# Kernel optimization log

Hardware: AMD Instinct MI355X
Metric: run time of the kernel (lower is better)

Reference implementation:

```python
import jax, jax.numpy as jnp
import numpy as np

V, H, FAST, SLOW = 32000, 256, 64, 256
B, T = 32, 1024
THRESH = 0.3
NEG = -1e9


def setup_inputs() -> dict:
    key = jax.random.key(0)
    ks = jax.random.split(key, 16)
    s = 0.02
    return {
        "seq":   jax.random.randint(ks[0], (B, T), 0, V),
        "embed": jax.random.normal(ks[1], (V, H), jnp.float32) * s,
        "W1": jax.random.normal(ks[2], (H, 2 * H), jnp.float32) * s,
        "b1": jnp.zeros((2 * H,), jnp.float32),
        "W2": jax.random.normal(ks[3], (2 * H, H), jnp.float32) * s,
        "b2": jnp.zeros((H,), jnp.float32),
        "gamma": jnp.ones((H,), jnp.float32),
        "beta":  jnp.zeros((H,), jnp.float32),
        "Wg": jax.random.normal(ks[4], (H, 1), jnp.float32) * s,
        "bg": jnp.zeros((1,), jnp.float32),
        "Wd": jax.random.normal(ks[5], (H, 1), jnp.float32) * s,
        "bd": jnp.zeros((1,), jnp.float32),
        "Wq": jax.random.normal(ks[6], (H, H), jnp.float32) * s,
        "bq": jnp.zeros((H,), jnp.float32),
        "Wo": jax.random.normal(ks[7], (H, V), jnp.float32) * s,
        "bo": jnp.zeros((V,), jnp.float32),
    }


def _layer_norm(x, g, b, eps=1e-5):
    mu = x.mean(-1, keepdims=True)
    var = ((x - mu) ** 2).mean(-1, keepdims=True)
    return (x - mu) * jax.lax.rsqrt(var + eps) * g + b


def _writer(h, Wg, bg, Wd, bd):
    """Vectorized-over-batch LRU writer with learned demotion; scan over time."""
    Bn = h.shape[0]
    init = (
        jnp.zeros((Bn, FAST, H), h.dtype),   # fast_mem
        jnp.zeros((Bn, SLOW, H), h.dtype),   # slow_mem
        jnp.zeros((Bn, FAST), jnp.int32),    # fast_age
        jnp.zeros((Bn, SLOW), jnp.int32),    # slow_age
        jnp.zeros((Bn, FAST), bool),         # fast_used
        jnp.zeros((Bn, SLOW), bool),         # slow_used
    )

    def step(st, tok_h):
        fm, sm, fa, sa, fu, su = st
        ws = jax.nn.sigmoid(tok_h @ Wg + bg)[:, 0]          # [B]
        fa = fa + fu.astype(jnp.int32)
        sa = sa + su.astype(jnp.int32)
        write = ws >= 0.4                                    # torch skips if < 0.4
        tok = jax.lax.stop_gradient(tok_h)                   # .detach() in torch

        free_f = ~fu                                         # [B,FAST]
        has_free = jnp.any(free_f, axis=1)                   # [B]
        sl = jnp.argmax(free_f, axis=1)                      # first free fast slot

        ds = (fm @ Wd + bd)[..., 0]                          # [B,FAST] demotion scores
        dem = jnp.argmin(ds, axis=1)                         # [B]
        dh = jnp.take_along_axis(fm, dem[:, None, None], axis=1)[:, 0]  # [B,H]

        free_s = ~su
        has_free_s = jnp.any(free_s, axis=1)
        ss = jnp.where(has_free_s, jnp.argmax(free_s, axis=1), jnp.argmax(sa, axis=1))

        fidx = jnp.where(has_free, sl, dem)                  # fast write slot
        sel_f = jax.nn.one_hot(fidx, FAST, dtype=bool) & write[:, None]
        do_slow = write & ~has_free                          # demotion happens
        sel_s = jax.nn.one_hot(ss, SLOW, dtype=bool) & do_slow[:, None]

        # slow write (demoted value) uses fm BEFORE the fast overwrite
        sm = jnp.where(sel_s[:, :, None], dh[:, None, :], sm)
        sa = jnp.where(sel_s, 0, sa)
        su = su | sel_s

        fm = jnp.where(sel_f[:, :, None], tok[:, None, :], fm)
        fa = jnp.where(sel_f, 0, fa)
        fu = fu | sel_f
        return (fm, sm, fa, sa, fu, su), None

    tokens = jnp.swapaxes(h[:, : h.shape[1] - 3], 0, 1)      # [T-3, B, H]
    (fm, sm, fa, sa, fu, su), _ = jax.lax.scan(step, init, tokens)
    return fm, sm, fu.astype(h.dtype), su.astype(h.dtype)


def reference(seq, embed, W1, b1, W2, b2, gamma, beta, Wg, bg, Wd, bd, Wq, bq, Wo, bo):
    h0 = embed[seq]                                          # [B,T,H]
    ff = jnp.maximum(h0 @ W1 + b1, 0.0) @ W2 + b2
    h = _layer_norm(h0 + ff, gamma, beta)

    fm, sm, fmask, smask = _writer(h, Wg, bg, Wd, bd)

    q = h[:, -1, :] @ Wq + bq                                # [B,H]
    f_scores = jnp.einsum("bfd,bd->bf", fm, q)
    f_scores = jnp.where(fmask == 0, NEG, f_scores)
    f_attn = jax.nn.softmax(f_scores, axis=-1)
    f_ctx = jnp.einsum("bf,bfd->bd", f_attn, fm)
    max_attn = f_attn.max(axis=-1)

    s_scores = jnp.einsum("bsd,bd->bs", sm, q)
    s_scores = jnp.where(smask == 0, NEG, s_scores)
    s_attn = jax.nn.softmax(s_scores, axis=-1)
    s_ctx = jnp.einsum("bs,bsd->bd", s_attn, sm)

    need_slow = (max_attn < THRESH).astype(h.dtype)          # [B]
    ctx = f_ctx + need_slow[:, None] * s_ctx
    logits = ctx @ Wo + bo
    return logits, need_slow
```

## Files before the change

### kernel.cpp

```cpp
#include <hip/hip_runtime.h>
#include <hip/hip_bf16.h>
#include <cstdint>

#define NEGV -1e9f

typedef __attribute__((ext_vector_type(8))) short short8v;
typedef __attribute__((ext_vector_type(4))) float f32x4;

union U8 {
  unsigned u[4];
  short8v v;
};

__device__ __forceinline__ float wred_sum(float v) {
#pragma unroll
  for (int o = 32; o; o >>= 1) v += __shfl_xor(v, o);
  return v;
}
__device__ __forceinline__ float wred_max(float v) {
#pragma unroll
  for (int o = 32; o; o >>= 1) v = fmaxf(v, __shfl_xor(v, o));
  return v;
}
template <int CTRL>
__device__ __forceinline__ float dpp_fadd(float x) {
  int xi = __float_as_int(x);
  int yi = __builtin_amdgcn_update_dpp(xi, xi, CTRL, 0xF, 0xF, false);
  return x + __int_as_float(yi);
}
__device__ __forceinline__ float dpp_sum63(float v) {
  v = dpp_fadd<0xB1>(v);
  v = dpp_fadd<0x4E>(v);
  v = dpp_fadd<0x141>(v);
  v = dpp_fadd<0x140>(v);
  v = dpp_fadd<0x142>(v);
  v = dpp_fadd<0x143>(v);
  return v;
}
__device__ __forceinline__ float dpp_sum16(float v) {
  v = dpp_fadd<0xB1>(v);
  v = dpp_fadd<0x4E>(v);
  v = dpp_fadd<0x141>(v);
  v = dpp_fadd<0x140>(v);
  return v;
}

__device__ __forceinline__ ushort bf16hi(float x) {
  unsigned u = __float_as_uint(x);
  unsigned r = u + 0x7FFFu + ((u >> 16) & 1u);
  return (ushort)(r >> 16);
}
__device__ __forceinline__ float bf16tof(ushort u) {
  return __uint_as_float(((unsigned)u) << 16);
}
__device__ __forceinline__ void split8(const float* xs, uint4& hv, uint4& lv) {
  unsigned h[8], l[8];
#pragma unroll
  for (int j = 0; j < 8; ++j) {
    const ushort hh = bf16hi(xs[j]);
    h[j] = hh;
    l[j] = bf16hi(xs[j] - bf16tof(hh));
  }
  hv = make_uint4(h[0] | (h[1] << 16), h[2] | (h[3] << 16),
                  h[4] | (h[5] << 16), h[6] | (h[7] << 16));
  lv = make_uint4(l[0] | (l[1] << 16), l[2] | (l[3] << 16),
                  l[4] | (l[5] << 16), l[6] | (l[7] << 16));
}

__device__ __forceinline__ void gload_lds16(const void* g, void* l) {
  __builtin_amdgcn_global_load_lds(
      (const __attribute__((address_space(1))) unsigned int*)g,
      (__attribute__((address_space(3))) unsigned int*)l, 16, 0, 0);
}

__global__ __launch_bounds__(256) void wprep2_k(const float* __restrict__ W,
                                                char* __restrict__ Wti, int K,
                                                int N) {
  __shared__ float tile[32][33];
  const int k0 = blockIdx.x * 32, n0 = blockIdx.y * 32;
  const int r = threadIdx.x >> 5, c = threadIdx.x & 31;
#pragma unroll
  for (int i = 0; i < 4; ++i)
    tile[r + i * 8][c] = W[(size_t)(k0 + r + i * 8) * N + n0 + c];
  __syncthreads();
  if (threadIdx.x < 128) {
    const int gn = threadIdx.x & 31, gk = threadIdx.x >> 5;
    float xs[8];
#pragma unroll
    for (int i = 0; i < 8; ++i) xs[i] = tile[gk * 8 + i][gn];
    uint4 hv, lv;
    split8(xs, hv, lv);
    char* dst = Wti + (size_t)(n0 + gn) * K * 4 + (k0 >> 5) * 128 + gk * 16;
    *(uint4*)dst = hv;
    *(uint4*)(dst + 64) = lv;
  }
}

__global__ __launch_bounds__(512, 2) void gemm1g_k(
    const int* __restrict__ seq, const float* __restrict__ embed,
    const char* __restrict__ w1ti, const float* __restrict__ bias,
    unsigned* __restrict__ outp) {
  __shared__ alignas(16) ushort A[4096];
  __shared__ alignas(16) ushort B[16384];
  __shared__ int sidx[64];
  const int tid = threadIdx.x;
  const int m0 = blockIdx.x * 64, n0 = blockIdx.y * 256;
  if (tid < 64) sidx[tid] = seq[m0 + tid];
  __syncthreads();
  const int lane = tid & 63, w = tid >> 6;
  const int wm = (w >> 2) * 32, wn = (w & 3) * 64;
  const int r15 = lane & 15, khalf = lane >> 4;

  f32x4 acc[2][4];
#pragma unroll
  for (int i = 0; i < 2; ++i)
#pragma unroll
    for (int j = 0; j < 4; ++j) acc[i][j] = (f32x4){0.f, 0.f, 0.f, 0.f};

#pragma unroll 1
  for (int s = 0; s < 8; ++s) {
    const size_t sb = (size_t)s * 128;
    if (tid < 256) {
      const int row = tid >> 2, q = tid & 3;
      const float* ap = embed + (size_t)sidx[row] * 256 + s * 32 + q * 8;
      const float4 x0 = *(const float4*)ap;
      const float4 x1 = *(const float4*)(ap + 4);
      const float xs[8] = {x0.x, x0.y, x0.z, x0.w, x1.x, x1.y, x1.z, x1.w};
      uint4 hv, lv;
      split8(xs, hv, lv);
      const int r7 = row & 7;
      *(uint4*)&A[(row * 8 + (q ^ r7)) * 8] = hv;
      *(uint4*)&A[(row * 8 + ((4 | q) ^ r7)) * 8] = lv;
    }
#pragma unroll
    for (int i = 0; i < 4; ++i) {
      const int cb = i * 512 + w * 64;
      const int c = cb + lane;
      const int row = c >> 3;
      const int lc = (c & 7) ^ (row & 7);
      gload_lds16(w1ti + (size_t)(n0 + row) * 1024 + sb + lc * 16,
                  &B[cb * 8]);
    }
    __syncthreads();
    short8v ahf[2], alf[2], bhf[4], blf[4];
#pragma unroll
    for (int t = 0; t < 2; ++t) {
      const int ra = wm + t * 16 + r15;
      ahf[t] = *(const short8v*)&A[(ra * 8 + (khalf ^ (ra & 7))) * 8];
      alf[t] = *(const short8v*)&A[(ra * 8 + ((4 | khalf) ^ (ra & 7))) * 8];
    }
#pragma unroll
    for (int t = 0; t < 4; ++t) {
      const int rb = wn + t * 16 + r15;
      bhf[t] = *(const short8v*)&B[(rb * 8 + (khalf ^ (rb & 7))) * 8];
      blf[t] = *(const short8v*)&B[(rb * 8 + ((4 | khalf) ^ (rb & 7))) * 8];
    }
#pragma unroll
    for (int mi = 0; mi < 2; ++mi)
#pragma unroll
      for (int ni = 0; ni < 4; ++ni) {
        acc[mi][ni] = __builtin_amdgcn_mfma_f32_16x16x32_bf16(
            ahf[mi], bhf[ni], acc[mi][ni], 0, 0, 0);
        acc[mi][ni] = __builtin_amdgcn_mfma_f32_16x16x32_bf16(
            ahf[mi], blf[ni], acc[mi][ni], 0, 0, 0);
        acc[mi][ni] = __builtin_amdgcn_mfma_f32_16x16x32_bf16(
            alf[mi], bhf[ni], acc[mi][ni], 0, 0, 0);
      }
    __syncthreads();
  }
#pragma unroll
  for (int ni = 0; ni < 4; ++ni) {
    const int n = n0 + wn + ni * 16 + r15;
    const float bv = bias[n];
#pragma unroll
    for (int mi = 0; mi < 2; ++mi) {
      const int mbase = m0 + wm + mi * 16 + khalf * 4;
#pragma unroll
      for (int j = 0; j < 4; ++j) {
        const float t = fmaxf(acc[mi][ni][j] + bv, 0.f);
        const ushort h = bf16hi(t);
        const ushort l = bf16hi(t - bf16tof(h));
        outp[(size_t)(mbase + j) * 512 + n] = (unsigned)h | ((unsigned)l << 16);
      }
    }
  }
}

__global__ __launch_bounds__(512, 2) void gemm2i_k(
    const unsigned* __restrict__ Ap, const char* __restrict__ w2ti,
    const float* __restrict__ b2, const int* __restrict__ seq,
    const float* __restrict__ embed, const float* __restrict__ gamma,
    const float* __restrict__ beta, const float* __restrict__ Wg,
    const float* __restrict__ bg, const float* __restrict__ Wd,
    const float* __restrict__ bd, float* __restrict__ X,
    int* __restrict__ wbit, float* __restrict__ dsc) {
  __shared__ alignas(16) unsigned Apk[2048];
  __shared__ alignas(16) ushort B[16384];
  __shared__ float par0[64][4], par1[64][4], gpar[64][4], dpar[64][4];
  __shared__ float g_s[256], be_s[256], wg_s[256], wd_s[256], b2_s[256];
  __shared__ int sidx[64];
  const int tid = threadIdx.x;
  const int m0 = blockIdx.x * 64;
  if (tid < 64) sidx[tid] = seq[m0 + tid];
  if (tid >= 256) {
    const int c = tid - 256;
    g_s[c] = gamma[c];
    be_s[c] = beta[c];
    wg_s[c] = Wg[c];
    wd_s[c] = Wd[c];
    b2_s[c] = b2[c];
  }
  const int lane = tid & 63, w = tid >> 6;
  const int wm = (w >> 2) * 32, wn = (w & 3) * 64;
  const int r15 = lane & 15, khalf = lane >> 4;

  f32x4 acc[2][4];
#pragma unroll
  for (int i = 0; i < 2; ++i)
#pragma unroll
    for (int j = 0; j < 4; ++j) acc[i][j] = (f32x4){0.f, 0.f, 0.f, 0.f};

#pragma unroll 1
  for (int s = 0; s < 16; ++s) {
    {
      const int cb = w * 64;
      const int c = cb + lane;
      const int row = c >> 3;
      const int lc = (c & 7) ^ (row & 7);
      gload_lds16(Ap + (size_t)(m0 + row) * 512 + s * 32 + lc * 4,
                  &Apk[cb * 4]);
    }
    const size_t sb = (size_t)s * 128;
#pragma unroll
    for (int i = 0; i < 4; ++i) {
      const int cb = i * 512 + w * 64;
      const int c = cb + lane;
      const int row = c >> 3;
      const int lc = (c & 7) ^ (row & 7);
      gload_lds16(w2ti + (size_t)row * 2048 + sb + lc * 16, &B[cb * 8]);
    }
    __syncthreads();
    short8v ahf[2], alf[2], bhf[4], blf[4];
#pragma unroll
    for (int t = 0; t < 2; ++t) {
      const int ra = wm + t * 16 + r15;
      const int r7 = ra & 7;
      const uint4 ua = *(const uint4*)&Apk[(ra * 8 + ((khalf * 2) ^ r7)) * 4];
      const uint4 ub =
          *(const uint4*)&Apk[(ra * 8 + ((khalf * 2 + 1) ^ r7)) * 4];
      U8 vh, vl;
      vh.u[0] = (ua.x & 0xffffu) | (ua.y << 16);
      vl.u[0] = (ua.x >> 16) | (ua.y & 0xffff0000u);
      vh.u[1] = (ua.z & 0xffffu) | (ua.w << 16);
      vl.u[1] = (ua.z >> 16) | (ua.w & 0xffff0000u);
      vh.u[2] = (ub.x & 0xffffu) | (ub.y << 16);
      vl.u[2] = (ub.x >> 16) | (ub.y & 0xffff0000u);
      vh.u[3] = (ub.z & 0xffffu) | (ub.w << 16);
      vl.u[3] = (ub.z >> 16) | (ub.w & 0xffff0000u);
      ahf[t] = vh.v;
      alf[t] = vl.v;
    }
#pragma unroll
    for (int t = 0; t < 4; ++t) {
      const int rb = wn + t * 16 + r15;
      bhf[t] = *(const short8v*)&B[(rb * 8 + (khalf ^ (rb & 7))) * 8];
      blf[t] = *(const short8v*)&B[(rb * 8 + ((4 | khalf) ^ (rb & 7))) * 8];
    }
#pragma unroll
    for (int mi = 0; mi < 2; ++mi)
#pragma unroll
      for (int ni = 0; ni < 4; ++ni) {
        acc[mi][ni] = __builtin_amdgcn_mfma_f32_16x16x32_bf16(
            ahf[mi], bhf[ni], acc[mi][ni], 0, 0, 0);
        acc[mi][ni] = __builtin_amdgcn_mfma_f32_16x16x32_bf16(
            ahf[mi], blf[ni], acc[mi][ni], 0, 0, 0);
        acc[mi][ni] = __builtin_amdgcn_mfma_f32_16x16x32_bf16(
            alf[mi], bhf[ni], acc[mi][ni], 0, 0, 0);
      }
    __syncthreads();
  }

  float mu_r[2][4];
#pragma unroll
  for (int mi = 0; mi < 2; ++mi)
#pragma unroll
    for (int j = 0; j < 4; ++j) {
      const int rowl = wm + mi * 16 + khalf * 4 + j;
      const float* ep = embed + (size_t)sidx[rowl] * 256;
#pragma unroll
      for (int ni = 0; ni < 4; ++ni) {
        const int col = wn + ni * 16 + r15;
        float t = acc[mi][ni][j] + b2_s[col];
        acc[mi][ni][j] = t + ep[col];
      }
      float s = (acc[mi][0][j] + acc[mi][1][j]) + (acc[mi][2][j] + acc[mi][3][j]);
      s = dpp_sum16(s);
      if (r15 == 0) par0[rowl][w & 3] = s;
    }
  __syncthreads();
#pragma unroll
  for (int mi = 0; mi < 2; ++mi)
#pragma unroll
    for (int j = 0; j < 4; ++j) {
      const int rowl = wm + mi * 16 + khalf * 4 + j;
      const float mu = ((par0[rowl][0] + par0[rowl][1]) +
                        (par0[rowl][2] + par0[rowl][3])) * (1.f / 256.f);
      mu_r[mi][j] = mu;
      const float d0 = acc[mi][0][j] - mu, d1 = acc[mi][1][j] - mu;
      const float d2 = acc[mi][2][j] - mu, d3 = acc[mi][3][j] - mu;
      float vv = (d0 * d0 + d1 * d1) + (d2 * d2 + d3 * d3);
      vv = dpp_sum16(vv);
      if (r15 == 0) par1[rowl][w & 3] = vv;
    }
  __syncthreads();
#pragma unroll
  for (int mi = 0; mi < 2; ++mi)
#pragma unroll
    for (int j = 0; j < 4; ++j) {
      const int rowl = wm + mi * 16 + khalf * 4 + j;
      const float mu = mu_r[mi][j];
      const float var = ((par1[rowl][0] + par1[rowl][1]) +
                         (par1[rowl][2] + par1[rowl][3])) * (1.f / 256.f);
      const float rstd = 1.f / sqrtf(var + 1e-5f);
      float ys[4], gw[4], dw[4];
#pragma unroll
      for (int ni = 0; ni < 4; ++ni) {
        const int col = wn + ni * 16 + r15;
        const float y = (acc[mi][ni][j] - mu) * rstd * g_s[col] + be_s[col];
        X[(size_t)(m0 + rowl) * 256 + col] = y;
        ys[ni] = y;
        gw[ni] = wg_s[col];
        dw[ni] = wd_s[col];
      }
      float gp = (ys[0] * gw[0] + ys[1] * gw[1]) + (ys[2] * gw[2] + ys[3] * gw[3]);
      float dp = (ys[0] * dw[0] + ys[1] * dw[1]) + (ys[2] * dw[2] + ys[3] * dw[3]);
      gp = dpp_sum16(gp);
      dp = dpp_sum16(dp);
      if (r15 == 0) {
        gpar[rowl][w & 3] = gp;
        dpar[rowl][w & 3] = dp;
      }
    }
  __syncthreads();
  if (tid < 64) {
    const int row = tid;
    const float gs = ((gpar[row][0] + gpar[row][1]) +
                      (gpar[row][2] + gpar[row][3])) + bg[0];
    const float dsv = ((dpar[row][0] + dpar[row][1]) +
                       (dpar[row][2] + dpar[row][3])) + bd[0];
    float sig;
    if (gs >= 0.f) {
      sig = 1.f / (1.f + expf(-gs));
    } else {
      const float e2 = expf(gs);
      sig = e2 / (1.f + e2);
    }
    wbit[m0 + row] = (sig >= 0.4f) ? 1 : 0;
    dsc[m0 + row] = dsv;
  }
}

__global__ __launch_bounds__(1024) void selattn_k(
    const int* __restrict__ wbit, const float* __restrict__ dsc,
    const float* __restrict__ X, const float* __restrict__ Wq,
    const float* __restrict__ bq, float* __restrict__ ctx,
    float* __restrict__ needs_out) {
  const int b = blockIdx.x;
  const int tid = threadIdx.x;
  const int lane = tid & 63, wv = tid >> 6;
  __shared__ unsigned long long skey[1024];
  __shared__ int stokl[1024];
  __shared__ int wavecnt[16];
  __shared__ int waveoff[17];
  __shared__ int fcnt_s[16], scnt_s[16];
  __shared__ int foff[16], soff[16];
  __shared__ int ft[64], st[256];
  __shared__ float hl[256], q[256];
  __shared__ float qpart[4][256];
  __shared__ float sc_f[64], at_f[64];
  __shared__ float sc_s[256], at_s[256];
  __shared__ float redm[4], reds[4];
  __shared__ float needs_s;
  __shared__ float cpart[16][256];

  const int t = tid;
  int flag = 0;
  float d = 0.f;
  if (t < 1021) {
    flag = wbit[b * 1024 + t];
    d = dsc[b * 1024 + t];
  }
  const unsigned long long m = __ballot(flag != 0);
  if (lane == 0) wavecnt[wv] = __popcll(m);
  skey[tid] = ~0ull;
  __syncthreads();
  if (tid == 0) {
    int acc = 0;
    for (int i = 0; i < 16; ++i) { waveoff[i] = acc; acc += wavecnt[i]; }
    waveoff[16] = acc;
  }
  __syncthreads();
  const int W = waveoff[16];
  if (flag) {
    unsigned u = __float_as_uint(d);
    u = (u & 0x80000000u) ? ~u : (u | 0x80000000u);
    const int w = waveoff[wv] + __popcll(m & ((1ull << lane) - 1ull));
    skey[w] = ((unsigned long long)u << 32) | (unsigned)w;
    stokl[w] = t;
  }
  __syncthreads();
  const unsigned long long ki = skey[tid];
  __syncthreads();
  if (tid == W - 1) skey[tid] = ~0ull;
  __syncthreads();

  const int K = W - 64;
  const int end2 = max(0, W - 257);
  int r1 = 0, r2 = 0;
#pragma unroll 16
  for (int j = 0; j < 1024; ++j) {
    const int lt = skey[j] < ki;
    r1 += lt;
    r2 += (j < end2) ? lt : 0;
  }
  bool fastf = false, slowf = false;
  if (tid < W) {
    const bool isLast = (tid == W - 1);
    const bool inEK = (!isLast) && (r1 < K);
    const bool inE2 = (tid < end2) && (r2 < K - 256);
    fastf = isLast || (!isLast && r1 >= K);
    slowf = inEK && !inE2;
  }

  const unsigned long long mf = __ballot(fastf);
  const unsigned long long ms = __ballot(slowf);
  if (lane == 0) { fcnt_s[wv] = __popcll(mf); scnt_s[wv] = __popcll(ms); }
  __syncthreads();
  if (tid == 0) {
    int a = 0, c = 0;
    for (int i = 0; i < 16; ++i) {
      foff[i] = a; a += fcnt_s[i];
      soff[i] = c; c += scnt_s[i];
    }
  }
  __syncthreads();
  if (fastf) {
    const int p = foff[wv] + __popcll(mf & ((1ull << lane) - 1ull));
    ft[p] = stokl[tid];
  }
  if (slowf) {
    const int p = soff[wv] + __popcll(ms & ((1ull << lane) - 1ull));
    st[p] = stokl[tid];
  }
  const int nf = min(W, 64);
  const int ns = min(max(K, 0), 256);

  const float* Xb = X + (size_t)b * 1024 * 256;
  if (tid < 256) hl[tid] = Xb[(size_t)1023 * 256 + tid];
  __syncthreads();

  {
    const int col = tid & 255, kc = tid >> 8;
    float a = 0.f;
    const float* wp = Wq + (size_t)(kc * 64) * 256 + col;
#pragma unroll 4
    for (int k = 0; k < 64; ++k) a = fmaf(hl[kc * 64 + k], wp[(size_t)k * 256], a);
    qpart[kc][col] = a;
  }
  __syncthreads();
  if (tid < 256)
    q[tid] = ((qpart[0][tid] + qpart[1][tid]) + qpart[2][tid]) + qpart[3][tid] +
             bq[tid];
  __syncthreads();

  const float4 qq = *(const float4*)(q + lane * 4);
#pragma unroll 2
  for (int i = 0; i < 20; ++i) {
    const int r = wv + 16 * i;
    bool valid;
    int tok;
    if (r < 64) { valid = r < nf; tok = valid ? ft[r] : 0; }
    else        { valid = (r - 64) < ns; tok = valid ? st[r - 64] : 0; }
    float sc = NEGV;
    if (valid) {
      const float4 xr = *(const float4*)(Xb + (size_t)tok * 256 + lane * 4);
      float p = (xr.x * qq.x + xr.y * qq.y) + (xr.z * qq.z + xr.w * qq.w);
      sc = dpp_sum63(p);
    }
    if (lane == 63) {
      if (r < 64) sc_f[r] = sc;
      else sc_s[r - 64] = sc;
    }
  }
  __syncthreads();

  if (wv < 4) {
    float s = sc_s[tid];
    float mx = wred_max(s);
    if (lane == 0) redm[wv] = mx;
  } else if (wv == 8) {
    float s = sc_f[lane];
    float mx = wred_max(s);
    float e = expf(s - mx);
    float sm = wred_sum(e);
    float a = e / sm;
    at_f[lane] = a;
    float ma = wred_max(a);
    if (lane == 0) needs_s = (ma < 0.3f) ? 1.f : 0.f;
  }
  __syncthreads();
  if (wv < 4) {
    float s = sc_s[tid];
    float mx = fmaxf(fmaxf(redm[0], redm[1]), fmaxf(redm[2], redm[3]));
    float e = expf(s - mx);
    float sm = wred_sum(e);
    if (lane == 0) reds[wv] = sm;
    at_s[tid] = e;
  }
  __syncthreads();
  if (tid < 256) {
    float sm = (reds[0] + reds[1]) + (reds[2] + reds[3]);
    at_s[tid] = at_s[tid] / sm;
  }
  __syncthreads();

  const float needs = needs_s;
  float4 cp = {0.f, 0.f, 0.f, 0.f};
#pragma unroll 2
  for (int i = 0; i < 20; ++i) {
    const int r = wv + 16 * i;
    bool valid;
    int tok;
    float a;
    if (r < 64) { valid = r < nf; tok = valid ? ft[r] : 0; a = at_f[r]; }
    else {
      valid = (r - 64) < ns;
      tok = valid ? st[r - 64] : 0;
      a = needs * at_s[r - 64];
    }
    if (valid) {
      const float4 xr = *(const float4*)(Xb + (size_t)tok * 256 + lane * 4);
      cp.x = fmaf(a, xr.x, cp.x);
      cp.y = fmaf(a, xr.y, cp.y);
      cp.z = fmaf(a, xr.z, cp.z);
      cp.w = fmaf(a, xr.w, cp.w);
    }
  }
  *(float4*)&cpart[wv][lane * 4] = cp;
  __syncthreads();
  if (tid < 256) {
    float c = 0.f;
#pragma unroll
    for (int w = 0; w < 16; ++w) c += cpart[w][tid];
    ctx[b * 256 + tid] = c;
  }
  if (tid == 0) needs_out[b] = needs;
}

__global__ __launch_bounds__(256) void logits5_k(
    const float* __restrict__ ctx, const float* __restrict__ Wo,
    const float* __restrict__ bo, float* __restrict__ out) {
  __shared__ float cs[256 * 8];
  const int tid = threadIdx.x;
  const int b0 = blockIdx.y * 8;
  for (int i = tid; i < 2048; i += 256) {
    int bb = i & 7, hh = i >> 3;
    cs[hh * 8 + bb] = ctx[(b0 + bb) * 256 + hh];
  }
  __syncthreads();
  const int v = blockIdx.x * 256 + tid;
  float acc[8] = {0.f, 0.f, 0.f, 0.f, 0.f, 0.f, 0.f, 0.f};
  for (int h0 = 0; h0 < 256; h0 += 16) {
    float wv[16];
#pragma unroll
    for (int u = 0; u < 16; ++u) wv[u] = Wo[(size_t)(h0 + u) * 32000 + v];
#pragma unroll
    for (int u = 0; u < 16; ++u) {
      const float4 c0 = *(const float4*)&cs[(h0 + u) * 8];
      const float4 c1 = *(const float4*)&cs[(h0 + u) * 8 + 4];
      acc[0] = fmaf(c0.x, wv[u], acc[0]);
      acc[1] = fmaf(c0.y, wv[u], acc[1]);
      acc[2] = fmaf(c0.z, wv[u], acc[2]);
      acc[3] = fmaf(c0.w, wv[u], acc[3]);
      acc[4] = fmaf(c1.x, wv[u], acc[4]);
      acc[5] = fmaf(c1.y, wv[u], acc[5]);
      acc[6] = fmaf(c1.z, wv[u], acc[6]);
      acc[7] = fmaf(c1.w, wv[u], acc[7]);
    }
  }
  const float bv = bo[v];
#pragma unroll
  for (int bb = 0; bb < 8; ++bb)
    out[(size_t)(b0 + bb) * 32000 + v] = acc[bb] + bv;
}

extern "C" void kernel_launch(void* const* d_in, const int* in_sizes, int n_in,
                              void* d_out, int out_size, void* d_ws,
                              size_t ws_size, hipStream_t stream) {
  const int* seq = (const int*)d_in[0];
  const float* embed = (const float*)d_in[1];
  const float* W1 = (const float*)d_in[2];
  const float* b1 = (const float*)d_in[3];
  const float* W2 = (const float*)d_in[4];
  const float* b2 = (const float*)d_in[5];
  const float* gamma = (const float*)d_in[6];
  const float* beta = (const float*)d_in[7];
  const float* Wg = (const float*)d_in[8];
  const float* bg = (const float*)d_in[9];
  const float* Wd = (const float*)d_in[10];
  const float* bd = (const float*)d_in[11];
  const float* Wq = (const float*)d_in[12];
  const float* bq = (const float*)d_in[13];
  const float* Wo = (const float*)d_in[14];
  const float* bo = (const float*)d_in[15];
  float* out = (float*)d_out;

  char* wsb = (char*)d_ws;
  char* w1ti = wsb;
  char* w2ti = wsb + 524288;
  int* wbit = (int*)(wsb + 1048576);
  float* dscp = (float*)(wsb + 1179648);
  float* ctxp = (float*)(wsb + 1310720);
  const size_t base = 1343488;

  const int nch = (ws_size >= (size_t)105000000) ? 1 : 2;
  const int rows = 32768 / nch;
  const size_t actsz = (size_t)rows * 512 * 4;
  unsigned* act1p = (unsigned*)(wsb + base);
  float* X = (float*)(wsb + base + actsz);

  dim3 blk(256);
  wprep2_k<<<dim3(8, 16), blk, 0, stream>>>(W1, w1ti, 256, 512);
  wprep2_k<<<dim3(16, 8), blk, 0, stream>>>(W2, w2ti, 512, 256);

  for (int c = 0; c < nch; ++c) {
    const int* seqc = seq + c * rows;
    gemm1g_k<<<dim3(rows / 64, 2), dim3(512), 0, stream>>>(seqc, embed, w1ti,
                                                           b1, act1p);
    gemm2i_k<<<dim3(rows / 64), dim3(512), 0, stream>>>(
        act1p, w2ti, b2, seqc, embed, gamma, beta, Wg, bg, Wd, bd,
        X + (size_t)c * rows * 256, wbit + c * rows, dscp + c * rows);
  }

  selattn_k<<<32, dim3(1024), 0, stream>>>(wbit, dscp, X, Wq, bq, ctxp,
                                           out + (size_t)32 * 32000);
  logits5_k<<<dim3(125, 4), blk, 0, stream>>>(ctxp, Wo, bo, out);
}
```

Before: 167.2 us.

## Split rank-counting loop into separate kernel parallelized across 8 slices per batch

Moves the O(N^2) rank computation for sorting write candidates out of selattn_k into a new rank_k kernel launched on an 8x32 grid. Each block counts over 128 keys and writes packed partial ranks, which selattn_k then sums. Only 32 blocks previously did the 1024-iteration LDS loop; spreading it over 256 blocks uses more CUs. In exchange it adds a kernel launch, recomputes the key compaction in every block, and uses extra workspace, which raises the single-chunk threshold.

```diff
diff --git a/kernel.cpp b/kernel.cpp
--- a/kernel.cpp
+++ b/kernel.cpp
@@ -360,15 +360,67 @@
   }
 }
 
+__global__ __launch_bounds__(1024) void rank_k(
+    const int* __restrict__ wbit, const float* __restrict__ dsc,
+    unsigned* __restrict__ r12) {
+  const int b = blockIdx.y;
+  const int s0 = blockIdx.x * 128;
+  const int tid = threadIdx.x;
+  const int lane = tid & 63, wv = tid >> 6;
+  __shared__ unsigned long long skey[1024];
+  __shared__ int wavecnt[16];
+  __shared__ int waveoff[17];
+
+  int flag = 0;
+  float d = 0.f;
+  if (tid < 1021) {
+    flag = wbit[b * 1024 + tid];
+    d = dsc[b * 1024 + tid];
+  }
+  const unsigned long long m = __ballot(flag != 0);
+  if (lane == 0) wavecnt[wv] = __popcll(m);
+  skey[tid] = ~0ull;
+  __syncthreads();
+  if (tid == 0) {
+    int acc = 0;
+    for (int i = 0; i < 16; ++i) { waveoff[i] = acc; acc += wavecnt[i]; }
+    waveoff[16] = acc;
+  }
+  __syncthreads();
+  const int W = waveoff[16];
+  if (flag) {
+    unsigned u = __float_as_uint(d);
+    u = (u & 0x80000000u) ? ~u : (u | 0x80000000u);
+    const int w = waveoff[wv] + __popcll(m & ((1ull << lane) - 1ull));
+    skey[w] = ((unsigned long long)u << 32) | (unsigned)w;
+  }
+  __syncthreads();
+  const unsigned long long ki = skey[tid];
+  __syncthreads();
+  if (tid == W - 1) skey[tid] = ~0ull;
+  __syncthreads();
+
+  const int end2 = max(0, W - 257);
+  int r1 = 0, r2 = 0;
+#pragma unroll 8
+  for (int jj = 0; jj < 128; ++jj) {
+    const int j = s0 + jj;
+    const int lt = skey[j] < ki;
+    r1 += lt;
+    r2 += (j < end2) ? lt : 0;
+  }
+  r12[((size_t)b * 8 + blockIdx.x) * 1024 + tid] =
+      (unsigned)r1 | ((unsigned)r2 << 16);
+}
+
 __global__ __launch_bounds__(1024) void selattn_k(
     const int* __restrict__ wbit, const float* __restrict__ dsc,
-    const float* __restrict__ X, const float* __restrict__ Wq,
-    const float* __restrict__ bq, float* __restrict__ ctx,
-    float* __restrict__ needs_out) {
+    const unsigned* __restrict__ r12, const float* __restrict__ X,
+    const float* __restrict__ Wq, const float* __restrict__ bq,
+    float* __restrict__ ctx, float* __restrict__ needs_out) {
   const int b = blockIdx.x;
   const int tid = threadIdx.x;
   const int lane = tid & 63, wv = tid >> 6;
-  __shared__ unsigned long long skey[1024];
   __shared__ int stokl[1024];
   __shared__ int wavecnt[16];
   __shared__ int waveoff[17];
@@ -383,16 +435,10 @@
   __shared__ float needs_s;
   __shared__ float cpart[16][256];
 
-  const int t = tid;
   int flag = 0;
-  float d = 0.f;
-  if (t < 1021) {
-    flag = wbit[b * 1024 + t];
-    d = dsc[b * 1024 + t];
-  }
+  if (tid < 1021) flag = wbit[b * 1024 + tid];
   const unsigned long long m = __ballot(flag != 0);
   if (lane == 0) wavecnt[wv] = __popcll(m);
-  skey[tid] = ~0ull;
   __syncthreads();
   if (tid == 0) {
     int acc = 0;
@@ -402,27 +448,23 @@
   __syncthreads();
   const int W = waveoff[16];
   if (flag) {
-    unsigned u = __float_as_uint(d);
-    u = (u & 0x80000000u) ? ~u : (u | 0x80000000u);
     const int w = waveoff[wv] + __popcll(m & ((1ull << lane) - 1ull));
-    skey[w] = ((unsigned long long)u << 32) | (unsigned)w;
-    stokl[w] = t;
-  }
-  __syncthreads();
-  const unsigned long long ki = skey[tid];
-  __syncthreads();
-  if (tid == W - 1) skey[tid] = ~0ull;
-  __syncthreads();
-
+    stokl[w] = tid;
+  }
+  __syncthreads();
+
+  int r1 = 0, r2 = 0;
+  {
+    const unsigned* rp = r12 + (size_t)b * 8192 + tid;
+#pragma unroll
+    for (int s = 0; s < 8; ++s) {
+      const unsigned v = rp[s * 1024];
+      r1 += (int)(v & 0xffffu);
+      r2 += (int)(v >> 16);
+    }
+  }
   const int K = W - 64;
   const int end2 = max(0, W - 257);
-  int r1 = 0, r2 = 0;
-#pragma unroll 16
-  for (int j = 0; j < 1024; ++j) {
-    const int lt = skey[j] < ki;
-    r1 += lt;
-    r2 += (j < end2) ? lt : 0;
-  }
   bool fastf = false, slowf = false;
   if (tid < W) {
     const bool isLast = (tid == W - 1);
@@ -621,9 +663,10 @@
   int* wbit = (int*)(wsb + 1048576);
   float* dscp = (float*)(wsb + 1179648);
   float* ctxp = (float*)(wsb + 1310720);
-  const size_t base = 1343488;
-
-  const int nch = (ws_size >= (size_t)105000000) ? 1 : 2;
+  unsigned* r12p = (unsigned*)(wsb + 1343488);
+  const size_t base = 2392064;
+
+  const int nch = (ws_size >= (size_t)106000000) ? 1 : 2;
   const int rows = 32768 / nch;
   const size_t actsz = (size_t)rows * 512 * 4;
   unsigned* act1p = (unsigned*)(wsb + base);
@@ -642,7 +685,8 @@
         X + (size_t)c * rows * 256, wbit + c * rows, dscp + c * rows);
   }
 
-  selattn_k<<<32, dim3(1024), 0, stream>>>(wbit, dscp, X, Wq, bq, ctxp,
+  rank_k<<<dim3(8, 32), dim3(1024), 0, stream>>>(wbit, dscp, r12p);
+  selattn_k<<<32, dim3(1024), 0, stream>>>(wbit, dscp, r12p, X, Wq, bq, ctxp,
                                            out + (size_t)32 * 32000);
   logits5_k<<<dim3(125, 4), blk, 0, stream>>>(ctxp, Wo, bo, out);
 }
```

After: 138.8 us, median of 2. -17.0%, faster.
